# Performance work log

Hardware: AMD Instinct MI355X
Metric: run time of the kernel (lower is better)

Reference implementation:

```python
import jax, jax.numpy as jnp
import numpy as np
from math import sqrt

HEADS = 16
D_MODEL = 1024
HEAD_DIM = D_MODEL // HEADS  # 64
B, SEQ = 2, 2048


def setup_inputs() -> dict:
    key = jax.random.key(0)
    ks = jax.random.split(key, 8)
    k = jax.random.normal(ks[0], (B, SEQ, D_MODEL), dtype=jnp.float32)
    q = jax.random.normal(ks[1], (B, SEQ, D_MODEL), dtype=jnp.float32)
    v = jax.random.normal(ks[2], (B, SEQ, D_MODEL), dtype=jnp.float32)
    # causal mask, broadcast over batch and heads; masked_fill where mask == 0
    mask = jnp.tril(jnp.ones((SEQ, SEQ), dtype=jnp.int32))[None, None, :, :]
    s = 1.0 / sqrt(HEAD_DIM)
    Wq = jax.random.normal(ks[3], (HEAD_DIM, HEAD_DIM), dtype=jnp.float32) * s
    Wk = jax.random.normal(ks[4], (HEAD_DIM, HEAD_DIM), dtype=jnp.float32) * s
    Wv = jax.random.normal(ks[5], (HEAD_DIM, HEAD_DIM), dtype=jnp.float32) * s
    Wo = jax.random.normal(ks[6], (D_MODEL, D_MODEL), dtype=jnp.float32) * (1.0 / sqrt(D_MODEL))
    bo = jax.random.normal(ks[7], (D_MODEL,), dtype=jnp.float32) * 0.01
    return {"key": k, "query": q, "value": v, "mask": mask,
            "Wq": Wq, "Wk": Wk, "Wv": Wv, "Wo": Wo, "bo": bo}


def reference(key, query, value, mask, Wq, Wk, Wv, Wo, bo):
    b, q_len, d = query.shape
    k_len = key.shape[1]
    hd = d // HEADS
    # reshape to [b, len, heads, head_dim]
    k = key.reshape(b, k_len, HEADS, hd)
    q = query.reshape(b, q_len, HEADS, hd)
    v = value.reshape(b, k_len, HEADS, hd)
    # per-head-dim Linear (weights shared across heads); torch Linear: y = x @ W.T
    k = jnp.einsum('bkhd,ed->bkhe', k, Wk)
    q = jnp.einsum('bqhd,ed->bqhe', q, Wq)
    v = jnp.einsum('bvhd,ed->bvhe', v, Wv)
    # full attention matrix [b, h, q, k]
    product = jnp.einsum('bqhd,bkhd->bhqk', q, k)
    # NOTE: original masks BEFORE scaling by 1/sqrt(head_dim)
    product = jnp.where(mask == 0, jnp.float32(-1e20), product)
    product = product / jnp.float32(sqrt(hd))
    score = jax.nn.softmax(product, axis=-1)
    out = jnp.einsum('bhqv,bvhd->bqhd', score, v).reshape(b, q_len, d)
    out = out @ Wo.T + bo
    return out
```

## Files before the change

kernel.cpp:

```cpp
#include <hip/hip_runtime.h>

typedef __bf16 bf16x8 __attribute__((ext_vector_type(8)));
typedef float  f32x4  __attribute__((ext_vector_type(4)));
typedef float  f32x16 __attribute__((ext_vector_type(16)));
typedef unsigned int uint32x4 __attribute__((ext_vector_type(4)));

#define MFMA16(a, b, c) __builtin_amdgcn_mfma_f32_16x16x32_bf16((a), (b), (c), 0, 0, 0)
#define MFMA32(a, b, c) __builtin_amdgcn_mfma_f32_32x32x16_bf16((a), (b), (c), 0, 0, 0)

#define CVTPK(d, x, y) asm("v_cvt_pk_bf16_f32 %0, %1, %2" : "=v"(d) : "v"(x), "v"(y))
#define PLSWAP(a, b)   asm("v_permlane32_swap_b32 %0, %1" : "+v"(a), "+v"(b))

constexpr int SEQ = 2048;
constexpr int DM  = 1024;
constexpr int NH  = 16;
constexpr int HD  = 64;
constexpr int BATCH = 2;

__device__ inline bf16x8 ld8_f32(const float* p) {
    f32x4 a = *(const f32x4*)p;
    f32x4 b = *(const f32x4*)(p + 4);
    bf16x8 r;
    r[0] = (__bf16)a[0]; r[1] = (__bf16)a[1]; r[2] = (__bf16)a[2]; r[3] = (__bf16)a[3];
    r[4] = (__bf16)b[0]; r[5] = (__bf16)b[1]; r[6] = (__bf16)b[2]; r[7] = (__bf16)b[3];
    return r;
}

__global__ __launch_bounds__(256)
void proj_kernel(const float* __restrict__ Xq, const float* __restrict__ Xk,
                 const float* __restrict__ Xv,
                 const float* __restrict__ Wq, const float* __restrict__ Wk,
                 const float* __restrict__ Wv,
                 __bf16* __restrict__ Qp, __bf16* __restrict__ Kp,
                 __bf16* __restrict__ Vp)
{
    const int tid  = threadIdx.x;
    const int w    = tid >> 6;
    const int lane = tid & 63;
    const int quad = lane >> 4;
    const int l16  = lane & 15;
    const int sblk = blockIdx.x;
    const int bh   = blockIdx.y;
    const int tz   = blockIdx.z;

    const float* X = (tz == 0) ? Xq : (tz == 1) ? Xk : Xv;
    const float* W = (tz == 0) ? Wq : (tz == 1) ? Wk : Wv;
    __bf16*      O = (tz == 0) ? Qp : (tz == 1) ? Kp : Vp;
    const float scale = (tz == 0) ? (0.125f * 1.44269504088896f) : 1.0f;

    const int b = bh >> 4, h = bh & 15;
    const int mrow = sblk * 64 + w * 16 + l16;

    const size_t xoff = (size_t)(b * SEQ + mrow) * DM + h * HD + quad * 8;
    bf16x8 a0 = ld8_f32(X + xoff);
    bf16x8 a1 = ld8_f32(X + xoff + 32);

    f32x4 acc[4];
    #pragma unroll
    for (int nt = 0; nt < 4; ++nt) {
        const size_t woff = (size_t)(nt * 16 + l16) * HD + quad * 8;
        bf16x8 b0 = ld8_f32(W + woff);
        bf16x8 b1 = ld8_f32(W + woff + 32);
        f32x4 c = {0.f, 0.f, 0.f, 0.f};
        c = MFMA16(a0, b0, c);
        c = MFMA16(a1, b1, c);
        acc[nt] = c;
    }

    __bf16* obase = O + (size_t)bh * SEQ * HD;
    #pragma unroll
    for (int nt = 0; nt < 4; ++nt) {
        #pragma unroll
        for (int r = 0; r < 4; ++r) {
            const int srow = sblk * 64 + w * 16 + quad * 4 + r;
            obase[(size_t)srow * HD + nt * 16 + l16] = (__bf16)(acc[nt][r] * scale);
        }
    }
}

__global__ __launch_bounds__(256, 2)
void attn_kernel(const __bf16* __restrict__ Qp, const __bf16* __restrict__ Kp,
                 const __bf16* __restrict__ Vp, __bf16* __restrict__ AO)
{
    __shared__ __align__(16) unsigned int K_lds[2][64 * 36];
    __shared__ __align__(16) unsigned int VT2[2][64 * 36];

    const int tid  = threadIdx.x;
    const int w    = tid >> 6;
    const int lane = tid & 63;
    const int hi   = lane >> 5;
    const int l32  = lane & 31;
    const int qg   = w >> 1;
    const int kg   = w & 1;
    const int pr   = blockIdx.x;
    const int bh   = blockIdx.y;

    const __bf16* Qb = Qp + (size_t)bh * SEQ * HD;
    const __bf16* Kb = Kp + (size_t)bh * SEQ * HD;
    const __bf16* Vb = Vp + (size_t)bh * SEQ * HD;

    const int krow = tid >> 3, kcol = tid & 7;
    const int jp = tid & 31, d0 = (tid >> 5) * 8;

    #pragma unroll
    for (int phase = 0; phase < 2; ++phase) {
        const int tile = (phase == 0) ? (31 - pr) : pr;
        const int q0   = tile * 64;
        const int nkc  = tile + 1;

        __syncthreads();

        const __bf16* qp = Qb + (size_t)(q0 + 32 * qg + l32) * HD + hi * 8;
        const bf16x8 qb0 = *(const bf16x8*)(qp);
        const bf16x8 qb1 = *(const bf16x8*)(qp + 16);
        const bf16x8 qb2 = *(const bf16x8*)(qp + 32);
        const bf16x8 qb3 = *(const bf16x8*)(qp + 48);

        f32x16 accO[2];
        #pragma unroll
        for (int et = 0; et < 2; ++et) {
            #pragma unroll
            for (int r = 0; r < 16; ++r) accO[et][r] = 0.f;
        }
        float rs0 = 0.f, rs1 = 0.f;

        uint32x4 kpre0 = *(const uint32x4*)(Kb + (size_t)krow * HD + kcol * 8);
        uint32x4 kpre1 = *(const uint32x4*)(Kb + (size_t)(krow + 32) * HD + kcol * 8);
        uint32x4 vlo   = *(const uint32x4*)(Vb + (size_t)(2 * jp) * HD + d0);
        uint32x4 vhi   = *(const uint32x4*)(Vb + (size_t)(2 * jp + 1) * HD + d0);

        for (int kc = 0; kc < nkc; ++kc) {
            const int buf = kc & 1;
            *(uint32x4*)&K_lds[buf][krow * 36 + kcol * 4]        = kpre0;
            *(uint32x4*)&K_lds[buf][(krow + 32) * 36 + kcol * 4] = kpre1;
            #pragma unroll
            for (int i2 = 0; i2 < 4; ++i2) {
                const unsigned int va = vlo[i2], vb = vhi[i2];
                VT2[buf][(d0 + 2 * i2    ) * 36 + jp] = (va & 0xffffu) | (vb << 16);
                VT2[buf][(d0 + 2 * i2 + 1) * 36 + jp] = (va >> 16) | (vb & 0xffff0000u);
            }
            __syncthreads();

            if (kc + 1 < nkc) {
                const size_t o = (size_t)(kc + 1) * 64;
                kpre0 = *(const uint32x4*)(Kb + (o + krow) * HD + kcol * 8);
                kpre1 = *(const uint32x4*)(Kb + (o + krow + 32) * HD + kcol * 8);
                vlo   = *(const uint32x4*)(Vb + (o + 2 * jp) * HD + d0);
                vhi   = *(const uint32x4*)(Vb + (o + 2 * jp + 1) * HD + d0);
            }

            if (!(kc == tile && qg == 0 && kg == 1)) {
                const __bf16* kp = (const __bf16*)&K_lds[buf][(32 * kg + l32) * 36] + hi * 8;
                f32x16 s;
                #pragma unroll
                for (int r = 0; r < 16; ++r) s[r] = 0.f;
                s = MFMA32(*(const bf16x8*)(kp),      qb0, s);
                s = MFMA32(*(const bf16x8*)(kp + 16), qb1, s);
                s = MFMA32(*(const bf16x8*)(kp + 32), qb2, s);
                s = MFMA32(*(const bf16x8*)(kp + 48), qb3, s);

                if (kc == tile && qg == kg) {
                    #pragma unroll
                    for (int r = 0; r < 16; ++r) {
                        const int cr = (r & 3) + 8 * (r >> 2) + 4 * hi;
                        if (cr > l32) s[r] = -1e30f;
                    }
                }

                float p[16];
                #pragma unroll
                for (int r = 0; r < 16; ++r) p[r] = exp2f(s[r]);
                #pragma unroll
                for (int r = 0; r < 8; ++r) { rs0 += p[2 * r]; rs1 += p[2 * r + 1]; }

                unsigned int w0, w1, w2, w3, w4, w5, w6, w7;
                CVTPK(w0, p[0],  p[1]);  CVTPK(w1, p[2],  p[3]);
                CVTPK(w2, p[4],  p[5]);  CVTPK(w3, p[6],  p[7]);
                CVTPK(w4, p[8],  p[9]);  CVTPK(w5, p[10], p[11]);
                CVTPK(w6, p[12], p[13]); CVTPK(w7, p[14], p[15]);
                PLSWAP(w0, w2); PLSWAP(w1, w3); PLSWAP(w4, w6); PLSWAP(w5, w7);
                uint32x4 u0 = {w0, w1, w2, w3};
                uint32x4 u1 = {w4, w5, w6, w7};
                const bf16x8 pa0 = *(const bf16x8*)&u0;
                const bf16x8 pa1 = *(const bf16x8*)&u1;

                #pragma unroll
                for (int et = 0; et < 2; ++et) {
                    const __bf16* vp = (const __bf16*)&VT2[buf][(et * 32 + l32) * 36]
                                       + 32 * kg + hi * 8;
                    accO[et] = MFMA32(pa0, *(const bf16x8*)(vp),      accO[et]);
                    accO[et] = MFMA32(pa1, *(const bf16x8*)(vp + 16), accO[et]);
                }
            }
        }

        __syncthreads();
        float* red = (float*)K_lds;
        float rsum = rs0 + rs1;
        if (kg == 1) {
            float* dst = red + (size_t)(qg * 64 + lane) * 33;
            #pragma unroll
            for (int r = 0; r < 16; ++r) { dst[r] = accO[0][r]; dst[16 + r] = accO[1][r]; }
            dst[32] = rsum;
        }
        __syncthreads();
        if (kg == 0) {
            const float* src = red + (size_t)(qg * 64 + lane) * 33;
            #pragma unroll
            for (int r = 0; r < 16; ++r) { accO[0][r] += src[r]; accO[1][r] += src[16 + r]; }
            rsum += src[32];
            const float rt  = rsum + __shfl_xor(rsum, 32, 64);
            const float ivq = 1.0f / rt;
            const int b = bh >> 4, h = bh & 15;
            #pragma unroll
            for (int r = 0; r < 16; ++r) {
                const int cr = (r & 3) + 8 * (r >> 2) + 4 * hi;
                const float iv = __shfl(ivq, cr, 64);
                __bf16* ao = AO + (size_t)(b * SEQ + q0 + 32 * qg + cr) * DM + h * HD;
                ao[l32]      = (__bf16)(accO[0][r] * iv);
                ao[32 + l32] = (__bf16)(accO[1][r] * iv);
            }
        }
    }
}

__global__ __launch_bounds__(256)
void wconv_kernel(const float* __restrict__ Wo, __bf16* __restrict__ Wb)
{
    const size_t i = ((size_t)blockIdx.x * 256 + threadIdx.x) * 8;
    *(bf16x8*)(Wb + i) = ld8_f32(Wo + i);
}

__global__ __launch_bounds__(256)
void ogemm_kernel(const __bf16* __restrict__ AO, const __bf16* __restrict__ Wb,
                  const float* __restrict__ bo, float* __restrict__ out)
{
    __shared__ __align__(16) unsigned int A_lds[2][64 * 36];
    __shared__ __align__(16) unsigned int B_lds[2][128 * 36];

    const int tid  = threadIdx.x;
    const int w    = tid >> 6;
    const int lane = tid & 63;
    const int quad = lane >> 4;
    const int l16  = lane & 15;
    const int m0   = blockIdx.x * 64;
    const int n0   = blockIdx.y * 128;

    const int row = tid >> 3, c = tid & 7;

    f32x4 acc[8];
    #pragma unroll
    for (int nt = 0; nt < 8; ++nt) { f32x4 z = {0.f,0.f,0.f,0.f}; acc[nt] = z; }

    uint32x4 apre[2], bpre[4];
    #pragma unroll
    for (int i = 0; i < 2; ++i)
        apre[i] = *(const uint32x4*)(AO + (size_t)(m0 + row + i * 32) * DM + c * 8);
    #pragma unroll
    for (int i = 0; i < 4; ++i)
        bpre[i] = *(const uint32x4*)(Wb + (size_t)(n0 + row + i * 32) * DM + c * 8);

    for (int kc = 0; kc < DM / 64; ++kc) {
        const int buf = kc & 1;
        #pragma unroll
        for (int i = 0; i < 2; ++i)
            *(uint32x4*)&A_lds[buf][(row + i * 32) * 36 + c * 4] = apre[i];
        #pragma unroll
        for (int i = 0; i < 4; ++i)
            *(uint32x4*)&B_lds[buf][(row + i * 32) * 36 + c * 4] = bpre[i];
        __syncthreads();

        if (kc + 1 < DM / 64) {
            const size_t o = (size_t)(kc + 1) * 64;
            #pragma unroll
            for (int i = 0; i < 2; ++i)
                apre[i] = *(const uint32x4*)(AO + (size_t)(m0 + row + i * 32) * DM + o + c * 8);
            #pragma unroll
            for (int i = 0; i < 4; ++i)
                bpre[i] = *(const uint32x4*)(Wb + (size_t)(n0 + row + i * 32) * DM + o + c * 8);
        }

        #pragma unroll
        for (int ks = 0; ks < 2; ++ks) {
            bf16x8 a = *(const bf16x8*)&A_lds[buf][(w * 16 + l16) * 36 + ks * 16 + quad * 4];
            #pragma unroll
            for (int nt = 0; nt < 8; ++nt) {
                bf16x8 bb = *(const bf16x8*)&B_lds[buf][(nt * 16 + l16) * 36 + ks * 16 + quad * 4];
                acc[nt] = MFMA16(a, bb, acc[nt]);
            }
        }
    }

    #pragma unroll
    for (int nt = 0; nt < 8; ++nt) {
        const int n = n0 + nt * 16 + l16;
        const float bof = bo[n];
        #pragma unroll
        for (int r = 0; r < 4; ++r) {
            const int m = m0 + w * 16 + quad * 4 + r;
            out[(size_t)m * DM + n] = acc[nt][r] + bof;
        }
    }
}

extern "C" void kernel_launch(void* const* d_in, const int* in_sizes, int n_in,
                              void* d_out, int out_size, void* d_ws, size_t ws_size,
                              hipStream_t stream)
{
    const float* key   = (const float*)d_in[0];
    const float* query = (const float*)d_in[1];
    const float* value = (const float*)d_in[2];
    const float* Wq = (const float*)d_in[4];
    const float* Wk = (const float*)d_in[5];
    const float* Wv = (const float*)d_in[6];
    const float* Wo = (const float*)d_in[7];
    const float* bo = (const float*)d_in[8];

    const size_t per = (size_t)BATCH * NH * SEQ * HD;
    __bf16* Qp = (__bf16*)d_ws;
    __bf16* Kp = Qp + per;
    __bf16* Vp = Kp + per;
    __bf16* AO = Vp + per;
    __bf16* Wb = Kp;

    proj_kernel<<<dim3(SEQ / 64, BATCH * NH, 3), 256, 0, stream>>>(
        query, key, value, Wq, Wk, Wv, Qp, Kp, Vp);
    attn_kernel<<<dim3(SEQ / 128, BATCH * NH), 256, 0, stream>>>(Qp, Kp, Vp, AO);
    wconv_kernel<<<dim3(DM * DM / (256 * 8)), 256, 0, stream>>>(Wo, Wb);
    ogemm_kernel<<<dim3(BATCH * SEQ / 64, DM / 128), 256, 0, stream>>>(
        AO, Wb, bo, (float*)d_out);
}
```

Measured before the change: 194.6 us.

## Deepen global prefetch to two stages with barriers that skip vmem waits

The attention and output-projection kernels now prefetch K/V and A/W tiles two iterations ahead, using two register sets with a manually unrolled pair of steps. The plain __syncthreads is replaced by an inline-asm barrier that waits only on LDS counters, so outstanding global loads keep running across the barrier. exp2f is swapped for the hardware exp2 builtin. This adds register pressure and relies on the compiler inserting correct vmcnt waits before the prefetched registers are used.

```diff
diff --git a/kernel.cpp b/kernel.cpp
--- a/kernel.cpp
+++ b/kernel.cpp
@@ -10,6 +10,16 @@
 
 #define CVTPK(d, x, y) asm("v_cvt_pk_bf16_f32 %0, %1, %2" : "=v"(d) : "v"(x), "v"(y))
 #define PLSWAP(a, b)   asm("v_permlane32_swap_b32 %0, %1" : "+v"(a), "+v"(b))
+
+#define BAR_KEEP_VMEM() asm volatile("s_waitcnt lgkmcnt(0)\n\ts_barrier" ::: "memory")
+
+__device__ inline float fast_exp2(float x) {
+#if __has_builtin(__builtin_amdgcn_exp2f)
+    return __builtin_amdgcn_exp2f(x);
+#else
+    return exp2f(x);
+#endif
+}
 
 constexpr int SEQ = 2048;
 constexpr int DM  = 1024;
@@ -124,29 +134,36 @@
         }
         float rs0 = 0.f, rs1 = 0.f;
 
-        uint32x4 kpre0 = *(const uint32x4*)(Kb + (size_t)krow * HD + kcol * 8);
-        uint32x4 kpre1 = *(const uint32x4*)(Kb + (size_t)(krow + 32) * HD + kcol * 8);
-        uint32x4 vlo   = *(const uint32x4*)(Vb + (size_t)(2 * jp) * HD + d0);
-        uint32x4 vhi   = *(const uint32x4*)(Vb + (size_t)(2 * jp + 1) * HD + d0);
-
-        for (int kc = 0; kc < nkc; ++kc) {
-            const int buf = kc & 1;
-            *(uint32x4*)&K_lds[buf][krow * 36 + kcol * 4]        = kpre0;
-            *(uint32x4*)&K_lds[buf][(krow + 32) * 36 + kcol * 4] = kpre1;
+        uint32x4 kA0, kA1, vAl, vAh, kB0, kB1, vBl, vBh;
+        kA0 = *(const uint32x4*)(Kb + (size_t)krow * HD + kcol * 8);
+        kA1 = *(const uint32x4*)(Kb + (size_t)(krow + 32) * HD + kcol * 8);
+        vAl = *(const uint32x4*)(Vb + (size_t)(2 * jp) * HD + d0);
+        vAh = *(const uint32x4*)(Vb + (size_t)(2 * jp + 1) * HD + d0);
+        if (nkc > 1) {
+            kB0 = *(const uint32x4*)(Kb + (size_t)(64 + krow) * HD + kcol * 8);
+            kB1 = *(const uint32x4*)(Kb + (size_t)(64 + krow + 32) * HD + kcol * 8);
+            vBl = *(const uint32x4*)(Vb + (size_t)(64 + 2 * jp) * HD + d0);
+            vBh = *(const uint32x4*)(Vb + (size_t)(64 + 2 * jp + 1) * HD + d0);
+        }
+
+        auto STEP = [&](int kc, int buf, uint32x4& kp0, uint32x4& kp1,
+                        uint32x4& vl, uint32x4& vh) {
+            *(uint32x4*)&K_lds[buf][krow * 36 + kcol * 4]        = kp0;
+            *(uint32x4*)&K_lds[buf][(krow + 32) * 36 + kcol * 4] = kp1;
             #pragma unroll
             for (int i2 = 0; i2 < 4; ++i2) {
-                const unsigned int va = vlo[i2], vb = vhi[i2];
+                const unsigned int va = vl[i2], vb = vh[i2];
                 VT2[buf][(d0 + 2 * i2    ) * 36 + jp] = (va & 0xffffu) | (vb << 16);
                 VT2[buf][(d0 + 2 * i2 + 1) * 36 + jp] = (va >> 16) | (vb & 0xffff0000u);
             }
-            __syncthreads();
-
-            if (kc + 1 < nkc) {
-                const size_t o = (size_t)(kc + 1) * 64;
-                kpre0 = *(const uint32x4*)(Kb + (o + krow) * HD + kcol * 8);
-                kpre1 = *(const uint32x4*)(Kb + (o + krow + 32) * HD + kcol * 8);
-                vlo   = *(const uint32x4*)(Vb + (o + 2 * jp) * HD + d0);
-                vhi   = *(const uint32x4*)(Vb + (o + 2 * jp + 1) * HD + d0);
+            BAR_KEEP_VMEM();
+
+            if (kc + 2 < nkc) {
+                const size_t o = (size_t)(kc + 2) * 64;
+                kp0 = *(const uint32x4*)(Kb + (o + krow) * HD + kcol * 8);
+                kp1 = *(const uint32x4*)(Kb + (o + krow + 32) * HD + kcol * 8);
+                vl  = *(const uint32x4*)(Vb + (o + 2 * jp) * HD + d0);
+                vh  = *(const uint32x4*)(Vb + (o + 2 * jp + 1) * HD + d0);
             }
 
             if (!(kc == tile && qg == 0 && kg == 1)) {
@@ -169,7 +186,7 @@
 
                 float p[16];
                 #pragma unroll
-                for (int r = 0; r < 16; ++r) p[r] = exp2f(s[r]);
+                for (int r = 0; r < 16; ++r) p[r] = fast_exp2(s[r]);
                 #pragma unroll
                 for (int r = 0; r < 8; ++r) { rs0 += p[2 * r]; rs1 += p[2 * r + 1]; }
 
@@ -192,6 +209,11 @@
                     accO[et] = MFMA32(pa1, *(const bf16x8*)(vp + 16), accO[et]);
                 }
             }
+        };
+
+        for (int kc = 0; kc < nkc; kc += 2) {
+            STEP(kc, 0, kA0, kA1, vAl, vAh);
+            if (kc + 1 < nkc) STEP(kc + 1, 1, kB0, kB1, vBl, vBh);
         }
 
         __syncthreads();
@@ -252,32 +274,35 @@
     #pragma unroll
     for (int nt = 0; nt < 8; ++nt) { f32x4 z = {0.f,0.f,0.f,0.f}; acc[nt] = z; }
 
-    uint32x4 apre[2], bpre[4];
-    #pragma unroll
-    for (int i = 0; i < 2; ++i)
-        apre[i] = *(const uint32x4*)(AO + (size_t)(m0 + row + i * 32) * DM + c * 8);
-    #pragma unroll
-    for (int i = 0; i < 4; ++i)
-        bpre[i] = *(const uint32x4*)(Wb + (size_t)(n0 + row + i * 32) * DM + c * 8);
-
-    for (int kc = 0; kc < DM / 64; ++kc) {
-        const int buf = kc & 1;
+    uint32x4 aA[2], bA[4], aB[2], bB[4];
+    #pragma unroll
+    for (int i = 0; i < 2; ++i) {
+        aA[i] = *(const uint32x4*)(AO + (size_t)(m0 + row + i * 32) * DM + c * 8);
+        aB[i] = *(const uint32x4*)(AO + (size_t)(m0 + row + i * 32) * DM + 64 + c * 8);
+    }
+    #pragma unroll
+    for (int i = 0; i < 4; ++i) {
+        bA[i] = *(const uint32x4*)(Wb + (size_t)(n0 + row + i * 32) * DM + c * 8);
+        bB[i] = *(const uint32x4*)(Wb + (size_t)(n0 + row + i * 32) * DM + 64 + c * 8);
+    }
+
+    auto GSTEP = [&](int kc, int buf, uint32x4 (&ap)[2], uint32x4 (&bp)[4]) {
         #pragma unroll
         for (int i = 0; i < 2; ++i)
-            *(uint32x4*)&A_lds[buf][(row + i * 32) * 36 + c * 4] = apre[i];
+            *(uint32x4*)&A_lds[buf][(row + i * 32) * 36 + c * 4] = ap[i];
         #pragma unroll
         for (int i = 0; i < 4; ++i)
-            *(uint32x4*)&B_lds[buf][(row + i * 32) * 36 + c * 4] = bpre[i];
-        __syncthreads();
-
-        if (kc + 1 < DM / 64) {
-            const size_t o = (size_t)(kc + 1) * 64;
+            *(uint32x4*)&B_lds[buf][(row + i * 32) * 36 + c * 4] = bp[i];
+        BAR_KEEP_VMEM();
+
+        if (kc + 2 < DM / 64) {
+            const size_t o = (size_t)(kc + 2) * 64;
             #pragma unroll
             for (int i = 0; i < 2; ++i)
-                apre[i] = *(const uint32x4*)(AO + (size_t)(m0 + row + i * 32) * DM + o + c * 8);
+                ap[i] = *(const uint32x4*)(AO + (size_t)(m0 + row + i * 32) * DM + o + c * 8);
             #pragma unroll
             for (int i = 0; i < 4; ++i)
-                bpre[i] = *(const uint32x4*)(Wb + (size_t)(n0 + row + i * 32) * DM + o + c * 8);
+                bp[i] = *(const uint32x4*)(Wb + (size_t)(n0 + row + i * 32) * DM + o + c * 8);
         }
 
         #pragma unroll
@@ -289,6 +314,11 @@
                 acc[nt] = MFMA16(a, bb, acc[nt]);
             }
         }
+    };
+
+    for (int kc = 0; kc < DM / 64; kc += 2) {
+        GSTEP(kc,     0, aA, bA);
+        GSTEP(kc + 1, 1, aB, bB);
     }
 
     #pragma unroll
```

Result: no change. 191.2 us (-1.7%).
